# Optimization experiments

Hardware: AMD Instinct MI355X
Metric: run time of the kernel (lower is better)

Reference implementation:

```python
import jax, jax.numpy as jnp
import numpy as np

WINDOW = 128
LOOK_BACKWARD = 1
LOOK_FORWARD = 0  # causal=True -> look_forward defaults to 0
THETA = 10000.0


def look_around(x, backward=LOOK_BACKWARD, forward=LOOK_FORWARD, pad_value=-1):
    # x: (b, w, n, ...). Pad along window axis, concat shifted slices along token axis.
    w = x.shape[1]
    pad_width = [(0, 0)] * x.ndim
    pad_width[1] = (backward, forward)
    padded = jnp.pad(x, pad_width, constant_values=pad_value)
    return jnp.concatenate([padded[:, i:i + w] for i in range(forward + backward + 1)], axis=2)


def rotate_half(x):
    x1, x2 = jnp.split(x, 2, axis=-1)
    return jnp.concatenate((-x2, x1), axis=-1)


def setup_inputs() -> dict:
    key = jax.random.key(0)
    kq, kk, kv = jax.random.split(key, 3)
    shape = (32, 4096, 64)
    return {
        "q": jax.random.normal(kq, shape, dtype=jnp.float32),
        "k": jax.random.normal(kk, shape, dtype=jnp.float32),
        "v": jax.random.normal(kv, shape, dtype=jnp.float32),
    }


def reference(q, k, v):
    b, n, d = q.shape
    scale = d ** -0.5
    w = n // WINDOW

    bq = q.reshape(b, w, WINDOW, d) * scale
    bk = look_around(k.reshape(b, w, WINDOW, d), pad_value=-1.0)
    bv = look_around(v.reshape(b, w, WINDOW, d), pad_value=-1.0)
    j = bk.shape[2]  # (1 + look_backward + look_forward) * WINDOW = 256

    # rotary pos emb (SinusoidalEmbeddings, no xpos -> scale = 1)
    inv_freq = 1.0 / (THETA ** (jnp.arange(0, d, 2, dtype=jnp.float32) / d))
    t = jnp.arange(j, dtype=jnp.float32)
    freqs = jnp.einsum('i,j->ij', t, inv_freq)
    freqs = jnp.concatenate((freqs, freqs), axis=-1)  # (j, d)
    q_freqs = freqs[-WINDOW:]  # queries align to the last WINDOW positions
    bq = bq * jnp.cos(q_freqs) + rotate_half(bq) * jnp.sin(q_freqs)
    bk = bk * jnp.cos(freqs) + rotate_half(bk) * jnp.sin(freqs)

    # position bookkeeping for masks
    seq = jnp.arange(n)
    b_t = seq.reshape(1, w, WINDOW)           # (1, w, i)
    bq_t = b_t[..., :, None]                  # (1, w, i, 1)
    bq_k = look_around(b_t, pad_value=-1)[..., None, :]  # (1, w, 1, j)
    pad_mask = bq_k == -1
    causal_mask = bq_t < bq_k

    sim = jnp.einsum('bwie,bwje->bwij', bq, bk)  # (b, w, i, j)
    mask_value = -jnp.finfo(sim.dtype).max
    sim = jnp.where(causal_mask | pad_mask, mask_value, sim)

    attn = jax.nn.softmax(sim, axis=-1)
    out = jnp.einsum('bwij,bwje->bwie', attn, bv)
    return out.reshape(b, n, d)
```

## Files before the change

### kernel.cpp

```cpp
#include <hip/hip_runtime.h>
#include <hip/hip_bf16.h>

#define BDIM 512

typedef __attribute__((ext_vector_type(8))) _Float16 f16x8;
typedef __attribute__((ext_vector_type(4))) _Float16 f16x4;
typedef __attribute__((ext_vector_type(4))) float f32x4;

#define EXP2F(x) __builtin_amdgcn_exp2f(x)

__global__ __launch_bounds__(512, 4)
void la_kernel(const float* __restrict__ qg, const float* __restrict__ kg,
               const float* __restrict__ vg, float* __restrict__ outg)
{
    __shared__ _Float16 Ks[2][128][72];
    __shared__ _Float16 Vt[2][64][140];

    const int wp = blockIdx.x, bb = blockIdx.y;
    const int tid = threadIdx.x;
    const int wv = tid >> 6, lane = tid & 63, g = lane >> 4, c = lane & 15;
    const int base = 256 * wp - 128;
    const float NEG = -3.0e38f;
    const float NLT32 = -0.28782313662425572f;
    const float QSCALE = 0.125f * 1.4426950408889634f;
    const size_t rowb = (size_t)bb * 4096;

    const int cbK = (tid & 7) << 2;
    float invfK[4];
    #pragma unroll
    for (int u = 0; u < 4; ++u) invfK[u] = __expf((float)(cbK + u) * NLT32);
    float invfQ[8];
    #pragma unroll
    for (int u = 0; u < 8; ++u) invfQ[u] = __expf((float)(8 * g + u) * NLT32);

    const int jqV = tid >> 4, eqV = tid & 15;
    const int colbV = ((jqV & 24) << 2) + 8 * (jqV & 3) + 4 * ((jqV >> 2) & 1);

    const int qrow = wv * 16 + c;

    auto stage = [&](int mm) {
        int sl = mm & 1;
        #pragma unroll
        for (int it = 0; it < 2; ++it) {
            int j = (tid + it * 512) >> 3;
            int t = 128 * mm + j;
            const float* p = kg + (rowb + base + t) * 64 + cbK;
            float4 x1 = *(const float4*)p;
            float4 x2 = *(const float4*)(p + 32);
            const float* x1p = &x1.x;
            const float* x2p = &x2.x;
            f16x4 lo, hi;
            #pragma unroll
            for (int u = 0; u < 4; ++u) {
                float sn, cs; __sincosf((float)t * invfK[u], &sn, &cs);
                lo[u] = (_Float16)(x1p[u] * cs - x2p[u] * sn);
                hi[u] = (_Float16)(x2p[u] * cs + x1p[u] * sn);
            }
            *(f16x4*)&Ks[sl][j][cbK]      = lo;
            *(f16x4*)&Ks[sl][j][cbK + 32] = hi;
        }
        float4 x[4];
        #pragma unroll
        for (int w = 0; w < 4; ++w)
            x[w] = *(const float4*)(vg + (rowb + base + 128 * mm + 4 * jqV + w) * 64 + 4 * eqV);
        #pragma unroll
        for (int u = 0; u < 4; ++u) {
            f16x4 o;
            o[0] = (_Float16)((const float*)&x[0])[u];
            o[1] = (_Float16)((const float*)&x[1])[u];
            o[2] = (_Float16)((const float*)&x[2])[u];
            o[3] = (_Float16)((const float*)&x[3])[u];
            *(f16x4*)&Vt[sl][4 * eqV + u][colbV] = o;
        }
    };

    auto loadQraw = [&](int wi, float4* qr) {
        const int tq = 128 * (wi + 1) + qrow;
        const float* p = qg + (rowb + base + tq) * 64 + 8 * g;
        qr[0] = *(const float4*)p;
        qr[1] = *(const float4*)(p + 4);
        qr[2] = *(const float4*)(p + 32);
        qr[3] = *(const float4*)(p + 36);
    };
    auto ropeQ = [&](int wi, const float4* qr, f16x8& qa0, f16x8& qa1) {
        const int tq = 128 * (wi + 1) + qrow;
        float ra[8] = {qr[0].x,qr[0].y,qr[0].z,qr[0].w,qr[1].x,qr[1].y,qr[1].z,qr[1].w};
        float rb[8] = {qr[2].x,qr[2].y,qr[2].z,qr[2].w,qr[3].x,qr[3].y,qr[3].z,qr[3].w};
        #pragma unroll
        for (int u = 0; u < 8; ++u) {
            float sn, cs; __sincosf((float)tq * invfQ[u], &sn, &cs);
            float a = ra[u] * QSCALE, b = rb[u] * QSCALE;
            qa0[u] = (_Float16)(a * cs - b * sn);
            qa1[u] = (_Float16)(b * cs + a * sn);
        }
    };

    auto computeWin = [&](int wi, f16x8 qa0, f16x8 qa1) {
        f32x4 accO[4];
        #pragma unroll
        for (int nt = 0; nt < 4; ++nt) accO[nt] = (f32x4){0.f,0.f,0.f,0.f};
        float m = NEG, s = 0.f;

        #pragma unroll 1
        for (int mm = wi; mm <= wi + 1; ++mm) {
            if (wp == 0 && mm == 0) continue;
            const int sl = mm & 1;
            const bool causal = (mm == wi + 1);

            #pragma unroll
            for (int ch = 0; ch < 2; ++ch) {
                if (causal && ch == 1 && wv < 4) continue;

                f32x4 acc[4];
                #pragma unroll
                for (int jt = 0; jt < 4; ++jt) acc[jt] = (f32x4){0.f,0.f,0.f,0.f};

                #pragma unroll
                for (int jt = 0; jt < 4; ++jt) {
                    int row = ch * 64 + jt * 16 + c;
                    f16x8 kb0 = *(const f16x8*)&Ks[sl][row][8 * g];
                    f16x8 kb1 = *(const f16x8*)&Ks[sl][row][32 + 8 * g];
                    acc[jt] = __builtin_amdgcn_mfma_f32_16x16x32_f16(kb0, qa0, acc[jt], 0, 0, 0);
                    acc[jt] = __builtin_amdgcn_mfma_f32_16x16x32_f16(kb1, qa1, acc[jt], 0, 0, 0);
                }

                if (causal) {
                    #pragma unroll
                    for (int jt = 0; jt < 4; ++jt)
                        #pragma unroll
                        for (int r = 0; r < 4; ++r) {
                            int jj = ch * 64 + jt * 16 + 4 * g + r;
                            if (jj > qrow) acc[jt][r] = NEG;
                        }
                }

                float mx = NEG;
                #pragma unroll
                for (int jt = 0; jt < 4; ++jt)
                    #pragma unroll
                    for (int r = 0; r < 4; ++r) mx = fmaxf(mx, acc[jt][r]);
                mx = fmaxf(mx, __shfl_xor(mx, 16));
                mx = fmaxf(mx, __shfl_xor(mx, 32));

                const bool grow = !__all(mx <= m);
                float mnew = grow ? fmaxf(m, mx) : m;

                float ps = 0.f;
                f16x8 pa[2];
                #pragma unroll
                for (int jt = 0; jt < 4; ++jt)
                    #pragma unroll
                    for (int r = 0; r < 4; ++r) {
                        float p = EXP2F(acc[jt][r] - mnew);
                        ps += p;
                        pa[jt >> 1][(jt & 1) * 4 + r] = (_Float16)p;
                    }
                ps += __shfl_xor(ps, 16);
                ps += __shfl_xor(ps, 32);

                if (grow) {
                    float alpha = EXP2F(m - mnew);
                    s = s * alpha + ps;
                    m = mnew;
                    float alphaD[4];
                    #pragma unroll
                    for (int r = 0; r < 4; ++r)
                        alphaD[r] = __shfl(alpha, (lane & 48) | (4 * g + r));
                    #pragma unroll
                    for (int nt = 0; nt < 4; ++nt)
                        #pragma unroll
                        for (int r = 0; r < 4; ++r) accO[nt][r] *= alphaD[r];
                } else {
                    s += ps;
                }

                #pragma unroll
                for (int st = 0; st < 2; ++st) {
                    #pragma unroll
                    for (int nt = 0; nt < 4; ++nt) {
                        f16x8 vb = *(const f16x8*)&Vt[sl][nt * 16 + c][ch * 64 + st * 32 + 8 * g];
                        accO[nt] = __builtin_amdgcn_mfma_f32_16x16x32_f16(pa[st], vb, accO[nt], 0, 0, 0);
                    }
                }
            }
        }

        float rcp = 1.0f / s;
        float rcpD[4];
        #pragma unroll
        for (int r = 0; r < 4; ++r)
            rcpD[r] = __shfl(rcp, (lane & 48) | (4 * g + r));

        float* op = outg + (rowb + base + 128 * (wi + 1) + wv * 16) * 64;
        #pragma unroll
        for (int nt = 0; nt < 4; ++nt)
            #pragma unroll
            for (int r = 0; r < 4; ++r)
                op[(size_t)(4 * g + r) * 64 + nt * 16 + c] = accO[nt][r] * rcpD[r];
    };

    float4 qr[4];
    loadQraw(0, qr);
    if (wp > 0) stage(0);
    stage(1);
    f16x8 qA, qB;
    ropeQ(0, qr, qA, qB);
    __syncthreads();
    computeWin(0, qA, qB);
    loadQraw(1, qr);
    __syncthreads();
    stage(2);
    ropeQ(1, qr, qA, qB);
    __syncthreads();
    computeWin(1, qA, qB);
}

extern "C" void kernel_launch(void* const* d_in, const int* in_sizes, int n_in,
                              void* d_out, int out_size, void* d_ws, size_t ws_size,
                              hipStream_t stream) {
    (void)in_sizes; (void)n_in; (void)out_size; (void)d_ws; (void)ws_size;
    const float* q = (const float*)d_in[0];
    const float* k = (const float*)d_in[1];
    const float* v = (const float*)d_in[2];
    float* out = (float*)d_out;
    dim3 grid(16, 32);
    la_kernel<<<grid, BDIM, 0, stream>>>(q, k, v, out);
}
```

Before: 33.24 us.

## Process one query window per block with single-buffered shared memory

Each block previously handled two consecutive query windows and reused the shared middle K/V window through double-buffered LDS. Now each block handles one window, staging the previous and current K/V windows one after another into a single LDS buffer, and the grid doubles to 32x32. Shared memory is halved and the launch bound is raised to 8 blocks, both aimed at higher occupancy and more parallelism. The cost is that each K/V window is loaded and rotated twice across blocks instead of once, and each block loses overlap between staging and compute.

```diff
diff --git a/kernel.cpp b/kernel.cpp
--- a/kernel.cpp
+++ b/kernel.cpp
@@ -9,21 +9,21 @@
 
 #define EXP2F(x) __builtin_amdgcn_exp2f(x)
 
-__global__ __launch_bounds__(512, 4)
+__global__ __launch_bounds__(512, 8)
 void la_kernel(const float* __restrict__ qg, const float* __restrict__ kg,
                const float* __restrict__ vg, float* __restrict__ outg)
 {
-    __shared__ _Float16 Ks[2][128][72];
-    __shared__ _Float16 Vt[2][64][140];
-
-    const int wp = blockIdx.x, bb = blockIdx.y;
+    __shared__ _Float16 Ks[128][72];
+    __shared__ _Float16 Vt[64][140];
+
+    const int ww = blockIdx.x, bb = blockIdx.y;
     const int tid = threadIdx.x;
     const int wv = tid >> 6, lane = tid & 63, g = lane >> 4, c = lane & 15;
-    const int base = 256 * wp - 128;
     const float NEG = -3.0e38f;
     const float NLT32 = -0.28782313662425572f;
     const float QSCALE = 0.125f * 1.4426950408889634f;
     const size_t rowb = (size_t)bb * 4096;
+    const int srow0 = ww * 128 - 128;
 
     const int cbK = (tid & 7) << 2;
     float invfK[4];
@@ -38,13 +38,12 @@
 
     const int qrow = wv * 16 + c;
 
-    auto stage = [&](int mm) {
-        int sl = mm & 1;
+    auto stage = [&](int h) {
         #pragma unroll
         for (int it = 0; it < 2; ++it) {
             int j = (tid + it * 512) >> 3;
-            int t = 128 * mm + j;
-            const float* p = kg + (rowb + base + t) * 64 + cbK;
+            int t = 128 * h + j;
+            const float* p = kg + (rowb + srow0 + t) * 64 + cbK;
             float4 x1 = *(const float4*)p;
             float4 x2 = *(const float4*)(p + 32);
             const float* x1p = &x1.x;
@@ -56,13 +55,13 @@
                 lo[u] = (_Float16)(x1p[u] * cs - x2p[u] * sn);
                 hi[u] = (_Float16)(x2p[u] * cs + x1p[u] * sn);
             }
-            *(f16x4*)&Ks[sl][j][cbK]      = lo;
-            *(f16x4*)&Ks[sl][j][cbK + 32] = hi;
+            *(f16x4*)&Ks[j][cbK]      = lo;
+            *(f16x4*)&Ks[j][cbK + 32] = hi;
         }
         float4 x[4];
         #pragma unroll
         for (int w = 0; w < 4; ++w)
-            x[w] = *(const float4*)(vg + (rowb + base + 128 * mm + 4 * jqV + w) * 64 + 4 * eqV);
+            x[w] = *(const float4*)(vg + (rowb + srow0 + 128 * h + 4 * jqV + w) * 64 + 4 * eqV);
         #pragma unroll
         for (int u = 0; u < 4; ++u) {
             f16x4 o;
@@ -70,149 +69,141 @@
             o[1] = (_Float16)((const float*)&x[1])[u];
             o[2] = (_Float16)((const float*)&x[2])[u];
             o[3] = (_Float16)((const float*)&x[3])[u];
-            *(f16x4*)&Vt[sl][4 * eqV + u][colbV] = o;
+            *(f16x4*)&Vt[4 * eqV + u][colbV] = o;
         }
     };
 
-    auto loadQraw = [&](int wi, float4* qr) {
-        const int tq = 128 * (wi + 1) + qrow;
-        const float* p = qg + (rowb + base + tq) * 64 + 8 * g;
+    f32x4 accO[4];
+    #pragma unroll
+    for (int nt = 0; nt < 4; ++nt) accO[nt] = (f32x4){0.f,0.f,0.f,0.f};
+    float m = NEG, s = 0.f;
+
+    auto computeHalf = [&](bool causal, f16x8 qa0, f16x8 qa1) {
+        #pragma unroll
+        for (int ch = 0; ch < 2; ++ch) {
+            if (causal && ch == 1 && wv < 4) continue;
+
+            f32x4 acc[4];
+            #pragma unroll
+            for (int jt = 0; jt < 4; ++jt) acc[jt] = (f32x4){0.f,0.f,0.f,0.f};
+
+            #pragma unroll
+            for (int jt = 0; jt < 4; ++jt) {
+                int row = ch * 64 + jt * 16 + c;
+                f16x8 kb0 = *(const f16x8*)&Ks[row][8 * g];
+                f16x8 kb1 = *(const f16x8*)&Ks[row][32 + 8 * g];
+                acc[jt] = __builtin_amdgcn_mfma_f32_16x16x32_f16(kb0, qa0, acc[jt], 0, 0, 0);
+                acc[jt] = __builtin_amdgcn_mfma_f32_16x16x32_f16(kb1, qa1, acc[jt], 0, 0, 0);
+            }
+
+            if (causal) {
+                #pragma unroll
+                for (int jt = 0; jt < 4; ++jt)
+                    #pragma unroll
+                    for (int r = 0; r < 4; ++r) {
+                        int jj = ch * 64 + jt * 16 + 4 * g + r;
+                        if (jj > qrow) acc[jt][r] = NEG;
+                    }
+            }
+
+            float mx = NEG;
+            #pragma unroll
+            for (int jt = 0; jt < 4; ++jt)
+                #pragma unroll
+                for (int r = 0; r < 4; ++r) mx = fmaxf(mx, acc[jt][r]);
+            mx = fmaxf(mx, __shfl_xor(mx, 16));
+            mx = fmaxf(mx, __shfl_xor(mx, 32));
+
+            const bool grow = !__all(mx <= m);
+            float mnew = grow ? fmaxf(m, mx) : m;
+
+            float ps = 0.f;
+            f16x8 pa[2];
+            #pragma unroll
+            for (int jt = 0; jt < 4; ++jt)
+                #pragma unroll
+                for (int r = 0; r < 4; ++r) {
+                    float p = EXP2F(acc[jt][r] - mnew);
+                    ps += p;
+                    pa[jt >> 1][(jt & 1) * 4 + r] = (_Float16)p;
+                }
+            ps += __shfl_xor(ps, 16);
+            ps += __shfl_xor(ps, 32);
+
+            if (grow) {
+                float alpha = EXP2F(m - mnew);
+                s = s * alpha + ps;
+                m = mnew;
+                float alphaD[4];
+                #pragma unroll
+                for (int r = 0; r < 4; ++r)
+                    alphaD[r] = __shfl(alpha, (lane & 48) | (4 * g + r));
+                #pragma unroll
+                for (int nt = 0; nt < 4; ++nt)
+                    #pragma unroll
+                    for (int r = 0; r < 4; ++r) accO[nt][r] *= alphaD[r];
+            } else {
+                s += ps;
+            }
+
+            #pragma unroll
+            for (int st = 0; st < 2; ++st) {
+                #pragma unroll
+                for (int nt = 0; nt < 4; ++nt) {
+                    f16x8 vb = *(const f16x8*)&Vt[nt * 16 + c][ch * 64 + st * 32 + 8 * g];
+                    accO[nt] = __builtin_amdgcn_mfma_f32_16x16x32_f16(pa[st], vb, accO[nt], 0, 0, 0);
+                }
+            }
+        }
+    };
+
+    float4 qr[4];
+    {
+        const float* p = qg + (rowb + ww * 128 + qrow) * 64 + 8 * g;
         qr[0] = *(const float4*)p;
         qr[1] = *(const float4*)(p + 4);
         qr[2] = *(const float4*)(p + 32);
         qr[3] = *(const float4*)(p + 36);
-    };
-    auto ropeQ = [&](int wi, const float4* qr, f16x8& qa0, f16x8& qa1) {
-        const int tq = 128 * (wi + 1) + qrow;
+    }
+
+    if (ww != 0) stage(0);
+
+    f16x8 qA, qB;
+    {
+        const float tq = (float)(128 + qrow);
         float ra[8] = {qr[0].x,qr[0].y,qr[0].z,qr[0].w,qr[1].x,qr[1].y,qr[1].z,qr[1].w};
         float rb[8] = {qr[2].x,qr[2].y,qr[2].z,qr[2].w,qr[3].x,qr[3].y,qr[3].z,qr[3].w};
         #pragma unroll
         for (int u = 0; u < 8; ++u) {
-            float sn, cs; __sincosf((float)tq * invfQ[u], &sn, &cs);
+            float sn, cs; __sincosf(tq * invfQ[u], &sn, &cs);
             float a = ra[u] * QSCALE, b = rb[u] * QSCALE;
-            qa0[u] = (_Float16)(a * cs - b * sn);
-            qa1[u] = (_Float16)(b * cs + a * sn);
-        }
-    };
-
-    auto computeWin = [&](int wi, f16x8 qa0, f16x8 qa1) {
-        f32x4 accO[4];
-        #pragma unroll
-        for (int nt = 0; nt < 4; ++nt) accO[nt] = (f32x4){0.f,0.f,0.f,0.f};
-        float m = NEG, s = 0.f;
-
-        #pragma unroll 1
-        for (int mm = wi; mm <= wi + 1; ++mm) {
-            if (wp == 0 && mm == 0) continue;
-            const int sl = mm & 1;
-            const bool causal = (mm == wi + 1);
-
-            #pragma unroll
-            for (int ch = 0; ch < 2; ++ch) {
-                if (causal && ch == 1 && wv < 4) continue;
-
-                f32x4 acc[4];
-                #pragma unroll
-                for (int jt = 0; jt < 4; ++jt) acc[jt] = (f32x4){0.f,0.f,0.f,0.f};
-
-                #pragma unroll
-                for (int jt = 0; jt < 4; ++jt) {
-                    int row = ch * 64 + jt * 16 + c;
-                    f16x8 kb0 = *(const f16x8*)&Ks[sl][row][8 * g];
-                    f16x8 kb1 = *(const f16x8*)&Ks[sl][row][32 + 8 * g];
-                    acc[jt] = __builtin_amdgcn_mfma_f32_16x16x32_f16(kb0, qa0, acc[jt], 0, 0, 0);
-                    acc[jt] = __builtin_amdgcn_mfma_f32_16x16x32_f16(kb1, qa1, acc[jt], 0, 0, 0);
-                }
-
-                if (causal) {
-                    #pragma unroll
-                    for (int jt = 0; jt < 4; ++jt)
-                        #pragma unroll
-                        for (int r = 0; r < 4; ++r) {
-                            int jj = ch * 64 + jt * 16 + 4 * g + r;
-                            if (jj > qrow) acc[jt][r] = NEG;
-                        }
-                }
-
-                float mx = NEG;
-                #pragma unroll
-                for (int jt = 0; jt < 4; ++jt)
-                    #pragma unroll
-                    for (int r = 0; r < 4; ++r) mx = fmaxf(mx, acc[jt][r]);
-                mx = fmaxf(mx, __shfl_xor(mx, 16));
-                mx = fmaxf(mx, __shfl_xor(mx, 32));
-
-                const bool grow = !__all(mx <= m);
-                float mnew = grow ? fmaxf(m, mx) : m;
-
-                float ps = 0.f;
-                f16x8 pa[2];
-                #pragma unroll
-                for (int jt = 0; jt < 4; ++jt)
-                    #pragma unroll
-                    for (int r = 0; r < 4; ++r) {
-                        float p = EXP2F(acc[jt][r] - mnew);
-                        ps += p;
-                        pa[jt >> 1][(jt & 1) * 4 + r] = (_Float16)p;
-                    }
-                ps += __shfl_xor(ps, 16);
-                ps += __shfl_xor(ps, 32);
-
-                if (grow) {
-                    float alpha = EXP2F(m - mnew);
-                    s = s * alpha + ps;
-                    m = mnew;
-                    float alphaD[4];
-                    #pragma unroll
-                    for (int r = 0; r < 4; ++r)
-                        alphaD[r] = __shfl(alpha, (lane & 48) | (4 * g + r));
-                    #pragma unroll
-                    for (int nt = 0; nt < 4; ++nt)
-                        #pragma unroll
-                        for (int r = 0; r < 4; ++r) accO[nt][r] *= alphaD[r];
-                } else {
-                    s += ps;
-                }
-
-                #pragma unroll
-                for (int st = 0; st < 2; ++st) {
-                    #pragma unroll
-                    for (int nt = 0; nt < 4; ++nt) {
-                        f16x8 vb = *(const f16x8*)&Vt[sl][nt * 16 + c][ch * 64 + st * 32 + 8 * g];
-                        accO[nt] = __builtin_amdgcn_mfma_f32_16x16x32_f16(pa[st], vb, accO[nt], 0, 0, 0);
-                    }
-                }
-            }
-        }
-
-        float rcp = 1.0f / s;
-        float rcpD[4];
+            qA[u] = (_Float16)(a * cs - b * sn);
+            qB[u] = (_Float16)(b * cs + a * sn);
+        }
+    }
+
+    if (ww != 0) {
+        __syncthreads();
+        computeHalf(false, qA, qB);
+        __syncthreads();
+    }
+
+    stage(1);
+    __syncthreads();
+    computeHalf(true, qA, qB);
+
+    float rcp = 1.0f / s;
+    float rcpD[4];
+    #pragma unroll
+    for (int r = 0; r < 4; ++r)
+        rcpD[r] = __shfl(rcp, (lane & 48) | (4 * g + r));
+
+    float* op = outg + (rowb + ww * 128 + wv * 16) * 64;
+    #pragma unroll
+    for (int nt = 0; nt < 4; ++nt)
         #pragma unroll
         for (int r = 0; r < 4; ++r)
-            rcpD[r] = __shfl(rcp, (lane & 48) | (4 * g + r));
-
-        float* op = outg + (rowb + base + 128 * (wi + 1) + wv * 16) * 64;
-        #pragma unroll
-        for (int nt = 0; nt < 4; ++nt)
-            #pragma unroll
-            for (int r = 0; r < 4; ++r)
-                op[(size_t)(4 * g + r) * 64 + nt * 16 + c] = accO[nt][r] * rcpD[r];
-    };
-
-    float4 qr[4];
-    loadQraw(0, qr);
-    if (wp > 0) stage(0);
-    stage(1);
-    f16x8 qA, qB;
-    ropeQ(0, qr, qA, qB);
-    __syncthreads();
-    computeWin(0, qA, qB);
-    loadQraw(1, qr);
-    __syncthreads();
-    stage(2);
-    ropeQ(1, qr, qA, qB);
-    __syncthreads();
-    computeWin(1, qA, qB);
+            op[(size_t)(4 * g + r) * 64 + nt * 16 + c] = accO[nt][r] * rcpD[r];
 }
 
 extern "C" void kernel_launch(void* const* d_in, const int* in_sizes, int n_in,
@@ -223,6 +214,6 @@
     const float* k = (const float*)d_in[1];
     const float* v = (const float*)d_in[2];
     float* out = (float*)d_out;
-    dim3 grid(16, 32);
+    dim3 grid(32, 32);
     la_kernel<<<grid, BDIM, 0, stream>>>(q, k, v, out);
 }
```

Result: slower. 39.19 us (+17.9%).

## Replace online softmax with single-pass full softmax over 256 keys with tile-level causal skip

Applied to the files above, without the earlier changes.

Each wave now computes all 16 score tiles (256 keys) into registers at once, takes one global row max, exponentiates, and does PV in a single pass, removing the online-softmax rescaling and its shuffles. Causal masking is done per 16-key tile: tiles beyond the wave's diagonal are skipped entirely and only the diagonal tile is masked. This raises register pressure (64 accumulator floats plus 8 P vectors) at 4 blocks of 512 threads, which risks spills or lower occupancy.

```diff
diff --git a/kernel.cpp b/kernel.cpp
--- a/kernel.cpp
+++ b/kernel.cpp
@@ -96,91 +96,77 @@
     };
 
     auto computeWin = [&](int wi, f16x8 qa0, f16x8 qa1) {
-        f32x4 accO[4];
-        #pragma unroll
-        for (int nt = 0; nt < 4; ++nt) accO[nt] = (f32x4){0.f,0.f,0.f,0.f};
-        float m = NEG, s = 0.f;
-
-        #pragma unroll 1
-        for (int mm = wi; mm <= wi + 1; ++mm) {
-            if (wp == 0 && mm == 0) continue;
-            const int sl = mm & 1;
-            const bool causal = (mm == wi + 1);
-
-            #pragma unroll
-            for (int ch = 0; ch < 2; ++ch) {
-                if (causal && ch == 1 && wv < 4) continue;
-
-                f32x4 acc[4];
-                #pragma unroll
-                for (int jt = 0; jt < 4; ++jt) acc[jt] = (f32x4){0.f,0.f,0.f,0.f};
-
-                #pragma unroll
-                for (int jt = 0; jt < 4; ++jt) {
-                    int row = ch * 64 + jt * 16 + c;
-                    f16x8 kb0 = *(const f16x8*)&Ks[sl][row][8 * g];
-                    f16x8 kb1 = *(const f16x8*)&Ks[sl][row][32 + 8 * g];
-                    acc[jt] = __builtin_amdgcn_mfma_f32_16x16x32_f16(kb0, qa0, acc[jt], 0, 0, 0);
-                    acc[jt] = __builtin_amdgcn_mfma_f32_16x16x32_f16(kb1, qa1, acc[jt], 0, 0, 0);
-                }
-
-                if (causal) {
-                    #pragma unroll
-                    for (int jt = 0; jt < 4; ++jt)
-                        #pragma unroll
-                        for (int r = 0; r < 4; ++r) {
-                            int jj = ch * 64 + jt * 16 + 4 * g + r;
-                            if (jj > qrow) acc[jt][r] = NEG;
-                        }
-                }
-
-                float mx = NEG;
-                #pragma unroll
-                for (int jt = 0; jt < 4; ++jt)
-                    #pragma unroll
-                    for (int r = 0; r < 4; ++r) mx = fmaxf(mx, acc[jt][r]);
-                mx = fmaxf(mx, __shfl_xor(mx, 16));
-                mx = fmaxf(mx, __shfl_xor(mx, 32));
-
-                const bool grow = !__all(mx <= m);
-                float mnew = grow ? fmaxf(m, mx) : m;
-
-                float ps = 0.f;
-                f16x8 pa[2];
-                #pragma unroll
-                for (int jt = 0; jt < 4; ++jt)
-                    #pragma unroll
-                    for (int r = 0; r < 4; ++r) {
-                        float p = EXP2F(acc[jt][r] - mnew);
-                        ps += p;
-                        pa[jt >> 1][(jt & 1) * 4 + r] = (_Float16)p;
-                    }
-                ps += __shfl_xor(ps, 16);
-                ps += __shfl_xor(ps, 32);
-
-                if (grow) {
-                    float alpha = EXP2F(m - mnew);
-                    s = s * alpha + ps;
-                    m = mnew;
-                    float alphaD[4];
+        const bool skipFirst = (wp == 0 && wi == 0);
+        const int sl0 = wi & 1, sl1 = (wi + 1) & 1;
+
+        f32x4 acc[16];
+        #pragma unroll
+        for (int jt = 0; jt < 16; ++jt) acc[jt] = (f32x4){0.f,0.f,0.f,0.f};
+
+        #pragma unroll
+        for (int jt = 0; jt < 16; ++jt) {
+            const bool doit = (jt < 8) ? (!skipFirst) : ((jt - 8) <= wv);
+            if (doit) {
+                const int sl = (jt < 8) ? sl0 : sl1;
+                const int row = (jt & 7) * 16 + c;
+                f16x8 kb0 = *(const f16x8*)&Ks[sl][row][8 * g];
+                f16x8 kb1 = *(const f16x8*)&Ks[sl][row][32 + 8 * g];
+                acc[jt] = __builtin_amdgcn_mfma_f32_16x16x32_f16(kb0, qa0, acc[jt], 0, 0, 0);
+                acc[jt] = __builtin_amdgcn_mfma_f32_16x16x32_f16(kb1, qa1, acc[jt], 0, 0, 0);
+            }
+        }
+
+        float mx = NEG;
+        #pragma unroll
+        for (int jt = 0; jt < 16; ++jt) {
+            const bool doit = (jt < 8) ? (!skipFirst) : ((jt - 8) <= wv);
+            if (doit) {
+                if (jt >= 8 && jt == 8 + wv) {
                     #pragma unroll
                     for (int r = 0; r < 4; ++r)
-                        alphaD[r] = __shfl(alpha, (lane & 48) | (4 * g + r));
-                    #pragma unroll
-                    for (int nt = 0; nt < 4; ++nt)
-                        #pragma unroll
-                        for (int r = 0; r < 4; ++r) accO[nt][r] *= alphaD[r];
-                } else {
-                    s += ps;
+                        if (4 * g + r > c) acc[jt][r] = NEG;
                 }
-
                 #pragma unroll
-                for (int st = 0; st < 2; ++st) {
-                    #pragma unroll
-                    for (int nt = 0; nt < 4; ++nt) {
-                        f16x8 vb = *(const f16x8*)&Vt[sl][nt * 16 + c][ch * 64 + st * 32 + 8 * g];
-                        accO[nt] = __builtin_amdgcn_mfma_f32_16x16x32_f16(pa[st], vb, accO[nt], 0, 0, 0);
-                    }
+                for (int r = 0; r < 4; ++r) mx = fmaxf(mx, acc[jt][r]);
+            }
+        }
+        mx = fmaxf(mx, __shfl_xor(mx, 16));
+        mx = fmaxf(mx, __shfl_xor(mx, 32));
+
+        f16x8 pa[8];
+        #pragma unroll
+        for (int p8 = 0; p8 < 8; ++p8)
+            pa[p8] = (f16x8){0.f,0.f,0.f,0.f,0.f,0.f,0.f,0.f};
+
+        float s = 0.f;
+        #pragma unroll
+        for (int jt = 0; jt < 16; ++jt) {
+            const bool doit = (jt < 8) ? (!skipFirst) : ((jt - 8) <= wv);
+            if (doit) {
+                #pragma unroll
+                for (int r = 0; r < 4; ++r) {
+                    float p = EXP2F(acc[jt][r] - mx);
+                    s += p;
+                    pa[jt >> 1][(jt & 1) * 4 + r] = (_Float16)p;
+                }
+            }
+        }
+        s += __shfl_xor(s, 16);
+        s += __shfl_xor(s, 32);
+
+        f32x4 accO[4];
+        #pragma unroll
+        for (int nt = 0; nt < 4; ++nt) accO[nt] = (f32x4){0.f,0.f,0.f,0.f};
+
+        #pragma unroll
+        for (int st = 0; st < 8; ++st) {
+            const bool doit = (st < 4) ? (!skipFirst) : ((2 * st - 8) <= wv);
+            if (doit) {
+                const int sl = (st < 4) ? sl0 : sl1;
+                #pragma unroll
+                for (int nt = 0; nt < 4; ++nt) {
+                    f16x8 vb = *(const f16x8*)&Vt[sl][nt * 16 + c][(st & 3) * 32 + 8 * g];
+                    accO[nt] = __builtin_amdgcn_mfma_f32_16x16x32_f16(pa[st], vb, accO[nt], 0, 0, 0);
                 }
             }
         }
```

Result: no change. 32.80 us (-1.3%).
